# Kernel tuning notes

Measured on AMD Instinct MI355X. Metric: run time of the kernel, lower is better.

The kernel has to match this reference:

```python
import jax, jax.numpy as jnp
import numpy as np

# PGA G(3,0,1) basis order: [1, e0, e1, e2, e3, e01, e02, e03, e12, e13, e23, e012, e013, e023, e123, e0123].
# The invariant inner product <rev(x) y>_0 only involves blades NOT containing e0; for those blades
# the metric contribution is +1, so it is a plain dot product over these 8 components.
_IP_IDX = np.array([0, 2, 3, 4, 8, 9, 10, 14])
_EPS = 1e-3  # config.normalizer_eps


def _normalizer(x):
    # _lin_square_normalizer: x / (x^2 + eps), a bounded ~1/x-style transform
    return x / (x * x + _EPS)


def setup_inputs() -> dict:
    key = jax.random.key(0)
    ks = jax.random.split(key, 7)
    B, H, N, CMV, CS = 2, 8, 2048, 16, 32
    f = lambda k, s: jax.random.normal(k, s, dtype=jnp.float32)
    return {
        "q_mv": f(ks[0], (B, H, N, CMV, 16)),
        "k_mv": f(ks[1], (B, H, N, CMV, 16)),
        "v_mv": f(ks[2], (B, H, N, CMV, 16)),
        "q_s": f(ks[3], (B, H, N, CS)),
        "k_s": f(ks[4], (B, H, N, CS)),
        "v_s": f(ks[5], (B, H, N, CS)),
        "log_weights": 0.1 * f(ks[6], (H, 1, CMV)),
    }


def reference(q_mv, k_mv, v_mv, q_s, k_s, v_s, log_weights):
    B, H, N, CMV, _ = q_mv.shape
    CS = q_s.shape[-1]

    # per-head, per-mv-channel learned positive weights, broadcast over items and blades
    w = jnp.exp(log_weights)[None, :, :, :, None]  # (1, H, 1, CMV, 1)

    # Term 1: weighted PGA inner product of multivector q/k (8 non-degenerate blades per channel)
    q_ip = (q_mv[..., _IP_IDX] * w).reshape(B, H, N, CMV * 8)
    k_ip = k_mv[..., _IP_IDX].reshape(B, H, N, CMV * 8)

    # Term 2: transformed scalar inner product <phi(q_s), psi(k_s)> with phi=psi=normalizer
    # Term 3: Euclidean scalar inner product <q_s, k_s>
    q_feat = jnp.concatenate([q_ip, _normalizer(q_s), q_s], axis=-1)  # (B,H,N, 8*CMV + 2*CS)
    k_feat = jnp.concatenate([k_ip, _normalizer(k_s), k_s], axis=-1)

    scale = 1.0 / jnp.sqrt(jnp.asarray(q_feat.shape[-1], dtype=q_feat.dtype))
    scores = jnp.einsum("bhid,bhjd->bhij", q_feat, k_feat) * scale  # (B,H,N,N)
    attn = jax.nn.softmax(scores, axis=-1)

    # Shared attention weights applied to flattened multivector + scalar values
    v_flat = jnp.concatenate([v_mv.reshape(B, H, N, CMV * 16), v_s], axis=-1)  # (B,H,N, 16*CMV+CS)
    out = jnp.einsum("bhij,bhjd->bhid", attn, v_flat)

    out_mv = out[..., : CMV * 16].reshape(B, H, N, CMV, 16)
    out_s = out[..., CMV * 16 :]
    return out_mv, out_s
```

## Files before the change

kernel.cpp:

```cpp
#include <hip/hip_runtime.h>

typedef float f32x4 __attribute__((ext_vector_type(4)));
typedef _Float16 f16x8 __attribute__((ext_vector_type(8)));
typedef _Float16 f16x4 __attribute__((ext_vector_type(4)));

#define NSEQ 2048
#define KVBLK 64
#define NITER (NSEQ / KVBLK)
#define KFBYTES (KVBLK * 384)
#define VTBYTES (288 * 2 * KVBLK)
#define TILEB (KFBYTES + VTBYTES)
#define KFOFF 0
#define VTOFF KFBYTES
#define PSTRIDE 72
#define WS_NEED (16ull * NITER * TILEB)

#define SCALE_L2E 0.10411754f
#define DEFER_THR 11.0f

__device__ __forceinline__ void async_copy16(const void* g, void* l) {
    __builtin_amdgcn_global_load_lds((const __attribute__((address_space(1))) unsigned int*)g,
                                     (__attribute__((address_space(3))) unsigned int*)l, 16, 0, 0);
}

__global__ __launch_bounds__(256)
void prep_kf(const float* __restrict__ k_mv, const float* __restrict__ k_s,
             unsigned char* __restrict__ ws)
{
    constexpr int IPIDX[8] = {0, 2, 3, 4, 8, 9, 10, 14};
    const int head = blockIdx.x >> 5, kt = blockIdx.x & 31;
    unsigned char* tb = ws + (size_t)(head * NITER + kt) * TILEB + KFOFF;
    const int tid = threadIdx.x;
    #pragma unroll
    for (int rep = 0; rep < 6; ++rep) {
        const int t = rep * 256 + tid;
        const int j = t & 63, oct = t >> 6;
        const size_t row = (size_t)head * NSEQ + kt * KVBLK + j;
        float v[8];
        if (oct < 16) {
            const float* p = k_mv + (row * 16 + oct) * 16;
            #pragma unroll
            for (int i = 0; i < 8; ++i) v[i] = p[IPIDX[i]];
        } else if (oct < 20) {
            const f32x4* p4 = (const f32x4*)(k_s + row * 32 + (oct - 16) * 8);
            f32x4 a = p4[0], b = p4[1];
            #pragma unroll
            for (int i = 0; i < 8; ++i) {
                float x = (i < 4) ? a[i & 3] : b[i & 3];
                v[i] = x / (x * x + 1e-3f);
            }
        } else {
            const f32x4* p4 = (const f32x4*)(k_s + row * 32 + (oct - 20) * 8);
            f32x4 a = p4[0], b = p4[1];
            #pragma unroll
            for (int i = 0; i < 8; ++i) v[i] = (i < 4) ? a[i & 3] : b[i & 3];
        }
        f16x8 o;
        #pragma unroll
        for (int i = 0; i < 8; ++i) o[i] = (_Float16)v[i];
        *(f16x8*)(tb + ((j * 384 + oct * 16) ^ ((j & 7) << 4))) = o;
    }
}

__global__ __launch_bounds__(256)
void prep_vt(const float* __restrict__ v_mv, const float* __restrict__ v_s,
             unsigned char* __restrict__ ws)
{
    const int head = blockIdx.x >> 5, kt = blockIdx.x & 31;
    unsigned char* tb = ws + (size_t)(head * NITER + kt) * TILEB + VTOFF;
    const int tid = threadIdx.x;
    const size_t row0 = (size_t)head * NSEQ + kt * KVBLK;
    {
        const int d = tid;
        float val[KVBLK];
        #pragma unroll
        for (int j = 0; j < KVBLK; ++j) val[j] = v_mv[(row0 + j) * 256 + d];
        #pragma unroll
        for (int jg = 0; jg < 8; ++jg) {
            f16x8 o;
            #pragma unroll
            for (int i = 0; i < 8; ++i) o[i] = (_Float16)val[jg * 8 + i];
            *(f16x8*)(tb + ((d * 128 + jg * 16) ^ ((d & 7) << 4))) = o;
        }
    }
    if (tid < 32) {
        const int d = 256 + tid;
        float val[KVBLK];
        #pragma unroll
        for (int j = 0; j < KVBLK; ++j) val[j] = v_s[(row0 + j) * 32 + tid];
        #pragma unroll
        for (int jg = 0; jg < 8; ++jg) {
            f16x8 o;
            #pragma unroll
            for (int i = 0; i < 8; ++i) o[i] = (_Float16)val[jg * 8 + i];
            *(f16x8*)(tb + ((d * 128 + jg * 16) ^ ((d & 7) << 4))) = o;
        }
    }
}

__global__ __launch_bounds__(256, 2)
void geoattn_main(const float* __restrict__ q_mv, const float* __restrict__ q_s,
                  const float* __restrict__ logw, const unsigned char* __restrict__ ws,
                  float* __restrict__ out)
{
    constexpr int IPIDX[8] = {0, 2, 3, 4, 8, 9, 10, 14};
    __shared__ __align__(16) unsigned char lbuf[TILEB];
    __shared__ __align__(16) _Float16 P_all[4][16 * PSTRIDE];

    const int bid  = blockIdx.x;
    const int head = (bid & 7) | ((bid >> 8) << 3);
    const int qt   = (bid >> 3) & 31;
    const int h    = head & 7;

    const int tid  = threadIdx.x;
    const int w    = tid >> 6;
    const int lane = tid & 63;
    const int lr   = lane & 15;
    const int lg   = lane >> 4;

    const size_t rowbase = (size_t)head * NSEQ;
    const int q0 = qt * 64;
    const unsigned char* wsh = ws + (size_t)head * NITER * TILEB;

    #pragma unroll
    for (int c = 0; c < 15; ++c)
        async_copy16(wsh + c * 4096 + tid * 16, &lbuf[c * 4096 + tid * 16]);

    f16x8 qf[6];
    {
        const int qrow = q0 + w * 16 + lr;
        const float* qmv = q_mv + (rowbase + qrow) * 256;
        const float* qs  = q_s  + (rowbase + qrow) * 32;
        #pragma unroll
        for (int c = 0; c < 4; ++c) {
            const int cmv = 4 * c + lg;
            const float wgt = __expf(logw[h * 16 + cmv]) * SCALE_L2E;
            const float* p = qmv + cmv * 16;
            #pragma unroll
            for (int i = 0; i < 8; ++i)
                qf[c][i] = (_Float16)(p[IPIDX[i]] * wgt);
        }
        const f32x4* p4 = (const f32x4*)(qs + lg * 8);
        f32x4 a = p4[0], b = p4[1];
        #pragma unroll
        for (int i = 0; i < 8; ++i) {
            float x = (i < 4) ? a[i & 3] : b[i & 3];
            qf[4][i] = (_Float16)(SCALE_L2E * x / (x * x + 1e-3f));
            qf[5][i] = (_Float16)(SCALE_L2E * x);
        }
    }

    f32x4 acc[18];
    #pragma unroll
    for (int dt = 0; dt < 18; ++dt) acc[dt] = f32x4{0.f, 0.f, 0.f, 0.f};
    float mrun = -1e30f, lrun = 0.f;

    _Float16* pb = &P_all[w][0];

    asm volatile("s_waitcnt vmcnt(0)" ::: "memory");
    __builtin_amdgcn_s_barrier();
    asm volatile("" ::: "memory");

    for (int kt = 0; kt < NITER; ++kt) {
        f32x4 sacc[4];
        #pragma unroll
        for (int jt = 0; jt < 4; ++jt) sacc[jt] = f32x4{0.f, 0.f, 0.f, 0.f};
        __builtin_amdgcn_s_setprio(1);
        #pragma unroll
        for (int jt = 0; jt < 4; ++jt) {
            const int j = jt * 16 + lr;
            #pragma unroll
            for (int c = 0; c < 6; ++c) {
                f16x8 kf = *(const f16x8*)(lbuf + KFOFF +
                            ((j * 384 + c * 64 + lg * 16) ^ ((lr & 7) << 4)));
                sacc[jt] = __builtin_amdgcn_mfma_f32_16x16x32_f16(kf, qf[c], sacc[jt], 0, 0, 0);
            }
        }
        __builtin_amdgcn_s_setprio(0);

        float mloc;
        {
            float t0 = fmaxf(fmaxf(sacc[0][0], sacc[0][1]), fmaxf(sacc[0][2], sacc[0][3]));
            #pragma unroll
            for (int jt = 1; jt < 4; ++jt) {
                float t1 = fmaxf(fmaxf(sacc[jt][0], sacc[jt][1]), fmaxf(sacc[jt][2], sacc[jt][3]));
                t0 = fmaxf(t0, t1);
            }
            t0 = fmaxf(t0, __shfl_xor(t0, 16));
            t0 = fmaxf(t0, __shfl_xor(t0, 32));
            mloc = t0;
        }
        const bool need = (mloc > mrun + DEFER_THR);
        const float mnew = need ? mloc : mrun;
        const float alpha = exp2f(mrun - mnew);
        mrun = mnew;
        if (__ballot(need)) {
            float ar[4];
            #pragma unroll
            for (int r = 0; r < 4; ++r) ar[r] = __shfl(alpha, lg * 4 + r, 16);
            #pragma unroll
            for (int dt = 0; dt < 18; ++dt)
                #pragma unroll
                for (int r = 0; r < 4; ++r) acc[dt][r] *= ar[r];
            lrun *= alpha;
        }
        float ps = 0.f;
        #pragma unroll
        for (int jt = 0; jt < 4; ++jt) {
            f16x4 pk;
            #pragma unroll
            for (int r = 0; r < 4; ++r) {
                const float p = exp2f(sacc[jt][r] - mrun);
                ps += p;
                pk[r] = (_Float16)p;
            }
            *(f16x4*)(&pb[lr * PSTRIDE + jt * 16 + lg * 4]) = pk;
        }
        ps += __shfl_xor(ps, 16);
        ps += __shfl_xor(ps, 32);
        lrun += ps;

        f16x8 pf0 = *(const f16x8*)(&pb[lr * PSTRIDE + lg * 8]);
        f16x8 pf1 = *(const f16x8*)(&pb[lr * PSTRIDE + 32 + lg * 8]);
        __builtin_amdgcn_s_setprio(1);
        #pragma unroll
        for (int dt = 0; dt < 18; ++dt) {
            const int d = dt * 16 + lr;
            const int vb = VTOFF + d * 128 + lg * 16;
            f16x8 vf0 = *(const f16x8*)(lbuf + ((vb) ^ ((d & 7) << 4)));
            f16x8 vf1 = *(const f16x8*)(lbuf + ((vb + 64) ^ ((d & 7) << 4)));
            acc[dt] = __builtin_amdgcn_mfma_f32_16x16x32_f16(pf0, vf0, acc[dt], 0, 0, 0);
            acc[dt] = __builtin_amdgcn_mfma_f32_16x16x32_f16(pf1, vf1, acc[dt], 0, 0, 0);
        }
        __builtin_amdgcn_s_setprio(0);

        asm volatile("s_waitcnt lgkmcnt(0)" ::: "memory");
        __builtin_amdgcn_s_barrier();
        asm volatile("" ::: "memory");
        if (kt < NITER - 1) {
            const unsigned char* src = wsh + (size_t)(kt + 1) * TILEB;
            #pragma unroll
            for (int c = 0; c < 15; ++c)
                async_copy16(src + c * 4096 + tid * 16, &lbuf[c * 4096 + tid * 16]);
            asm volatile("s_waitcnt vmcnt(0)" ::: "memory");
            __builtin_amdgcn_s_barrier();
            asm volatile("" ::: "memory");
        }
    }

    #pragma unroll
    for (int r = 0; r < 4; ++r) {
        const float lv = __shfl(lrun, lg * 4 + r, 16);
        const float inv = 1.0f / lv;
        const int row = q0 + w * 16 + lg * 4 + r;
        float* omv = out + (rowbase + row) * 256;
        float* os  = out + 8388608ull + (rowbase + row) * 32;
        #pragma unroll
        for (int dt = 0; dt < 18; ++dt) {
            const int d = dt * 16 + lr;
            const float val = acc[dt][r] * inv;
            if (d < 256) omv[d] = val;
            else         os[d - 256] = val;
        }
    }
}

#define FKSTRIDE 200
#define FVSTRIDE 72
__global__ __launch_bounds__(256, 2)
void geoattn_fallback(const float* __restrict__ q_mv, const float* __restrict__ k_mv,
                      const float* __restrict__ v_mv, const float* __restrict__ q_s,
                      const float* __restrict__ k_s, const float* __restrict__ v_s,
                      const float* __restrict__ logw, float* __restrict__ out)
{
    constexpr int IPIDX[8] = {0, 2, 3, 4, 8, 9, 10, 14};
    __shared__ __align__(16) _Float16 lds_k[64 * FKSTRIDE];
    __shared__ __align__(16) _Float16 lds_vt[288 * FVSTRIDE];
    __shared__ __align__(16) _Float16 lds_p[4 * 16 * FVSTRIDE];

    const int bid  = blockIdx.x;
    const int head = (bid & 7) | ((bid >> 8) << 3);
    const int qt   = (bid >> 3) & 31;
    const int h    = head & 7;
    const int tid  = threadIdx.x;
    const int w    = tid >> 6;
    const int lane = tid & 63;
    const int lr   = lane & 15;
    const int lg   = lane >> 4;
    const size_t rowbase = (size_t)head * NSEQ;
    const int q0 = qt * 64;
    const float scale = 0.07216878364870323f;

    f16x8 qf[6];
    {
        const int qrow = q0 + w * 16 + lr;
        const float* qmv = q_mv + (rowbase + qrow) * 256;
        const float* qs  = q_s  + (rowbase + qrow) * 32;
        #pragma unroll
        for (int c = 0; c < 4; ++c) {
            const int cmv = 4 * c + lg;
            const float wgt = __expf(logw[h * 16 + cmv]) * scale;
            const float* p = qmv + cmv * 16;
            #pragma unroll
            for (int i = 0; i < 8; ++i) qf[c][i] = (_Float16)(p[IPIDX[i]] * wgt);
        }
        const f32x4* p4 = (const f32x4*)(qs + lg * 8);
        f32x4 a = p4[0], b = p4[1];
        #pragma unroll
        for (int i = 0; i < 8; ++i) {
            float x = (i < 4) ? a[i & 3] : b[i & 3];
            qf[4][i] = (_Float16)(scale * x / (x * x + 1e-3f));
            qf[5][i] = (_Float16)(scale * x);
        }
    }
    f32x4 acc[18];
    #pragma unroll
    for (int dt = 0; dt < 18; ++dt) acc[dt] = f32x4{0.f, 0.f, 0.f, 0.f};
    float mrun[4] = {-1e30f, -1e30f, -1e30f, -1e30f};
    float lrun[4] = {0.f, 0.f, 0.f, 0.f};

    for (int kt = 0; kt < 32; ++kt) {
        const int j0 = kt * 64;
        __syncthreads();
        #pragma unroll
        for (int rep = 0; rep < 6; ++rep) {
            const int t = rep * 256 + tid;
            const int j = t & 63, oct = t >> 6;
            const size_t krow = rowbase + j0 + j;
            float v[8];
            if (oct < 16) {
                const float* p = k_mv + (krow * 16 + oct) * 16;
                #pragma unroll
                for (int i = 0; i < 8; ++i) v[i] = p[IPIDX[i]];
            } else if (oct < 20) {
                const f32x4* p4 = (const f32x4*)(k_s + krow * 32 + (oct - 16) * 8);
                f32x4 a = p4[0], b = p4[1];
                #pragma unroll
                for (int i = 0; i < 8; ++i) {
                    float x = (i < 4) ? a[i & 3] : b[i & 3];
                    v[i] = x / (x * x + 1e-3f);
                }
            } else {
                const f32x4* p4 = (const f32x4*)(k_s + krow * 32 + (oct - 20) * 8);
                f32x4 a = p4[0], b = p4[1];
                #pragma unroll
                for (int i = 0; i < 8; ++i) v[i] = (i < 4) ? a[i & 3] : b[i & 3];
            }
            f16x8 o;
            #pragma unroll
            for (int i = 0; i < 8; ++i) o[i] = (_Float16)v[i];
            *(f16x8*)(&lds_k[j * FKSTRIDE + oct * 8]) = o;
        }
        #pragma unroll
        for (int rep = 0; rep < 9; ++rep) {
            const int t = rep * 256 + tid;
            const int j = t & 63, oct = t >> 6;
            const size_t vrow = rowbase + j0 + j;
            const float* src = (oct < 32) ? (v_mv + vrow * 256 + oct * 8)
                                          : (v_s  + vrow * 32 + (oct - 32) * 8);
            const f32x4* p4 = (const f32x4*)src;
            f32x4 a = p4[0], b = p4[1];
            const int d0 = oct * 8;
            #pragma unroll
            for (int i = 0; i < 8; ++i)
                lds_vt[(d0 + i) * FVSTRIDE + j] = (_Float16)((i < 4) ? a[i & 3] : b[i & 3]);
        }
        __syncthreads();
        f32x4 sacc[4];
        #pragma unroll
        for (int nt = 0; nt < 4; ++nt) {
            sacc[nt] = f32x4{0.f, 0.f, 0.f, 0.f};
            #pragma unroll
            for (int c = 0; c < 6; ++c) {
                f16x8 kf = *(const f16x8*)(&lds_k[(lr + 16 * nt) * FKSTRIDE + 32 * c + lg * 8]);
                sacc[nt] = __builtin_amdgcn_mfma_f32_16x16x32_f16(qf[c], kf, sacc[nt], 0, 0, 0);
            }
        }
        float tmax[4], alpha[4];
        #pragma unroll
        for (int r = 0; r < 4; ++r) {
            float t0 = fmaxf(fmaxf(sacc[0][r], sacc[1][r]), fmaxf(sacc[2][r], sacc[3][r]));
            #pragma unroll
            for (int mm = 1; mm < 16; mm <<= 1) t0 = fmaxf(t0, __shfl_xor(t0, mm));
            tmax[r] = t0;
        }
        bool need = false;
        #pragma unroll
        for (int r = 0; r < 4; ++r) {
            float mnew = fmaxf(mrun[r], tmax[r]);
            need = need || (tmax[r] > mrun[r]);
            alpha[r] = __expf(mrun[r] - mnew);
            mrun[r] = mnew;
        }
        float pvv[4][4];
        float psum[4] = {0.f, 0.f, 0.f, 0.f};
        #pragma unroll
        for (int nt = 0; nt < 4; ++nt)
            #pragma unroll
            for (int r = 0; r < 4; ++r) {
                float p = __expf(sacc[nt][r] - mrun[r]);
                pvv[nt][r] = p;
                psum[r] += p;
            }
        #pragma unroll
        for (int r = 0; r < 4; ++r) {
            float s = psum[r];
            #pragma unroll
            for (int mm = 1; mm < 16; mm <<= 1) s += __shfl_xor(s, mm);
            lrun[r] = lrun[r] * alpha[r] + s;
        }
        if (__ballot(need)) {
            #pragma unroll
            for (int dt = 0; dt < 18; ++dt)
                #pragma unroll
                for (int r = 0; r < 4; ++r) acc[dt][r] *= alpha[r];
        }
        _Float16* pbf = &lds_p[w * 16 * FVSTRIDE];
        #pragma unroll
        for (int nt = 0; nt < 4; ++nt)
            #pragma unroll
            for (int r = 0; r < 4; ++r)
                pbf[(lg * 4 + r) * FVSTRIDE + lr + 16 * nt] = (_Float16)pvv[nt][r];
        #pragma unroll
        for (int ch = 0; ch < 2; ++ch) {
            f16x8 pf = *(const f16x8*)(&pbf[lr * FVSTRIDE + 32 * ch + lg * 8]);
            #pragma unroll
            for (int dt = 0; dt < 18; ++dt) {
                f16x8 vf = *(const f16x8*)(&lds_vt[(lr + 16 * dt) * FVSTRIDE + 32 * ch + lg * 8]);
                acc[dt] = __builtin_amdgcn_mfma_f32_16x16x32_f16(pf, vf, acc[dt], 0, 0, 0);
            }
        }
    }
    const int orow = q0 + w * 16 + lg * 4;
    #pragma unroll
    for (int r = 0; r < 4; ++r) {
        const float inv = 1.0f / lrun[r];
        float* omv = out + (rowbase + orow + r) * 256;
        float* os  = out + 8388608ull + (rowbase + orow + r) * 32;
        #pragma unroll
        for (int dt = 0; dt < 18; ++dt) {
            const int d = lr + 16 * dt;
            const float val = acc[dt][r] * inv;
            if (d < 256) omv[d] = val;
            else         os[d - 256] = val;
        }
    }
}

extern "C" void kernel_launch(void* const* d_in, const int* in_sizes, int n_in,
                              void* d_out, int out_size, void* d_ws, size_t ws_size,
                              hipStream_t stream) {
    (void)in_sizes; (void)n_in; (void)out_size;
    const float* q_mv = (const float*)d_in[0];
    const float* k_mv = (const float*)d_in[1];
    const float* v_mv = (const float*)d_in[2];
    const float* q_s  = (const float*)d_in[3];
    const float* k_s  = (const float*)d_in[4];
    const float* v_s  = (const float*)d_in[5];
    const float* logw = (const float*)d_in[6];
    float* out = (float*)d_out;

    if (ws_size >= WS_NEED) {
        unsigned char* ws = (unsigned char*)d_ws;
        prep_kf<<<dim3(512), dim3(256), 0, stream>>>(k_mv, k_s, ws);
        prep_vt<<<dim3(512), dim3(256), 0, stream>>>(v_mv, v_s, ws);
        geoattn_main<<<dim3(512), dim3(256), 0, stream>>>(q_mv, q_s, logw, ws, out);
    } else {
        geoattn_fallback<<<dim3(512), dim3(256), 0, stream>>>(q_mv, k_mv, v_mv, q_s, k_s, v_s, logw, out);
    }
}
```

Baseline: 122.6 us.

## Stream V tiles from global into registers and keep only K in LDS

The main kernel now stages only the K-feature tile in LDS and loads the transposed V tile straight from global memory (L2) into registers, in three chunks spread across the QK, softmax and PV phases. The prefetch of the next K tile now starts right after the QK MFMAs instead of at the end of the iteration. The V layout in the workspace drops its XOR swizzle to match the direct global reads. This shrinks LDS per block and overlaps V fetch latency with compute, at the cost of many more vector registers for the V fragments and a reliance on L2 hits for V, since each head's V is reread by 32 query-tile blocks.

```diff
diff --git a/kernel.cpp b/kernel.cpp
--- a/kernel.cpp
+++ b/kernel.cpp
@@ -80,7 +80,7 @@
             f16x8 o;
             #pragma unroll
             for (int i = 0; i < 8; ++i) o[i] = (_Float16)val[jg * 8 + i];
-            *(f16x8*)(tb + ((d * 128 + jg * 16) ^ ((d & 7) << 4))) = o;
+            *(f16x8*)(tb + d * 128 + jg * 16) = o;
         }
     }
     if (tid < 32) {
@@ -93,7 +93,7 @@
             f16x8 o;
             #pragma unroll
             for (int i = 0; i < 8; ++i) o[i] = (_Float16)val[jg * 8 + i];
-            *(f16x8*)(tb + ((d * 128 + jg * 16) ^ ((d & 7) << 4))) = o;
+            *(f16x8*)(tb + d * 128 + jg * 16) = o;
         }
     }
 }
@@ -104,7 +104,7 @@
                   float* __restrict__ out)
 {
     constexpr int IPIDX[8] = {0, 2, 3, 4, 8, 9, 10, 14};
-    __shared__ __align__(16) unsigned char lbuf[TILEB];
+    __shared__ __align__(16) unsigned char lbuf[KFBYTES];
     __shared__ __align__(16) _Float16 P_all[4][16 * PSTRIDE];
 
     const int bid  = blockIdx.x;
@@ -123,8 +123,8 @@
     const unsigned char* wsh = ws + (size_t)head * NITER * TILEB;
 
     #pragma unroll
-    for (int c = 0; c < 15; ++c)
-        async_copy16(wsh + c * 4096 + tid * 16, &lbuf[c * 4096 + tid * 16]);
+    for (int c = 0; c < 6; ++c)
+        async_copy16(wsh + KFOFF + c * 4096 + tid * 16, &lbuf[c * 4096 + tid * 16]);
 
     f16x8 qf[6];
     {
@@ -157,11 +157,21 @@
 
     _Float16* pb = &P_all[w][0];
 
-    asm volatile("s_waitcnt vmcnt(0)" ::: "memory");
-    __builtin_amdgcn_s_barrier();
-    asm volatile("" ::: "memory");
-
     for (int kt = 0; kt < NITER; ++kt) {
+        asm volatile("s_waitcnt vmcnt(0)" ::: "memory");
+        __builtin_amdgcn_s_barrier();
+        asm volatile("" ::: "memory");
+
+        const unsigned char* vtile = wsh + (size_t)kt * TILEB + VTOFF;
+
+        f16x8 vA[6][2];
+        #pragma unroll
+        for (int dl = 0; dl < 6; ++dl) {
+            const int d = dl * 16 + lr;
+            vA[dl][0] = *(const f16x8*)(vtile + d * 128 + lg * 16);
+            vA[dl][1] = *(const f16x8*)(vtile + d * 128 + 64 + lg * 16);
+        }
+
         f32x4 sacc[4];
         #pragma unroll
         for (int jt = 0; jt < 4; ++jt) sacc[jt] = f32x4{0.f, 0.f, 0.f, 0.f};
@@ -177,6 +187,23 @@
             }
         }
         __builtin_amdgcn_s_setprio(0);
+
+        asm volatile("s_waitcnt lgkmcnt(0)" ::: "memory");
+        __builtin_amdgcn_s_barrier();
+        asm volatile("" ::: "memory");
+        if (kt < NITER - 1) {
+            const unsigned char* src = wsh + (size_t)(kt + 1) * TILEB + KFOFF;
+            #pragma unroll
+            for (int c = 0; c < 6; ++c)
+                async_copy16(src + c * 4096 + tid * 16, &lbuf[c * 4096 + tid * 16]);
+        }
+        f16x8 vB[6][2];
+        #pragma unroll
+        for (int dl = 0; dl < 6; ++dl) {
+            const int d = (6 + dl) * 16 + lr;
+            vB[dl][0] = *(const f16x8*)(vtile + d * 128 + lg * 16);
+            vB[dl][1] = *(const f16x8*)(vtile + d * 128 + 64 + lg * 16);
+        }
 
         float mloc;
         {
@@ -224,28 +251,30 @@
         f16x8 pf1 = *(const f16x8*)(&pb[lr * PSTRIDE + 32 + lg * 8]);
         __builtin_amdgcn_s_setprio(1);
         #pragma unroll
-        for (int dt = 0; dt < 18; ++dt) {
-            const int d = dt * 16 + lr;
-            const int vb = VTOFF + d * 128 + lg * 16;
-            f16x8 vf0 = *(const f16x8*)(lbuf + ((vb) ^ ((d & 7) << 4)));
-            f16x8 vf1 = *(const f16x8*)(lbuf + ((vb + 64) ^ ((d & 7) << 4)));
-            acc[dt] = __builtin_amdgcn_mfma_f32_16x16x32_f16(pf0, vf0, acc[dt], 0, 0, 0);
-            acc[dt] = __builtin_amdgcn_mfma_f32_16x16x32_f16(pf1, vf1, acc[dt], 0, 0, 0);
+        for (int dl = 0; dl < 6; ++dl) {
+            acc[dl] = __builtin_amdgcn_mfma_f32_16x16x32_f16(pf0, vA[dl][0], acc[dl], 0, 0, 0);
+            acc[dl] = __builtin_amdgcn_mfma_f32_16x16x32_f16(pf1, vA[dl][1], acc[dl], 0, 0, 0);
         }
         __builtin_amdgcn_s_setprio(0);
-
-        asm volatile("s_waitcnt lgkmcnt(0)" ::: "memory");
-        __builtin_amdgcn_s_barrier();
-        asm volatile("" ::: "memory");
-        if (kt < NITER - 1) {
-            const unsigned char* src = wsh + (size_t)(kt + 1) * TILEB;
-            #pragma unroll
-            for (int c = 0; c < 15; ++c)
-                async_copy16(src + c * 4096 + tid * 16, &lbuf[c * 4096 + tid * 16]);
-            asm volatile("s_waitcnt vmcnt(0)" ::: "memory");
-            __builtin_amdgcn_s_barrier();
-            asm volatile("" ::: "memory");
-        }
+        f16x8 vC[6][2];
+        #pragma unroll
+        for (int dl = 0; dl < 6; ++dl) {
+            const int d = (12 + dl) * 16 + lr;
+            vC[dl][0] = *(const f16x8*)(vtile + d * 128 + lg * 16);
+            vC[dl][1] = *(const f16x8*)(vtile + d * 128 + 64 + lg * 16);
+        }
+        __builtin_amdgcn_s_setprio(1);
+        #pragma unroll
+        for (int dl = 0; dl < 6; ++dl) {
+            acc[6 + dl] = __builtin_amdgcn_mfma_f32_16x16x32_f16(pf0, vB[dl][0], acc[6 + dl], 0, 0, 0);
+            acc[6 + dl] = __builtin_amdgcn_mfma_f32_16x16x32_f16(pf1, vB[dl][1], acc[6 + dl], 0, 0, 0);
+        }
+        #pragma unroll
+        for (int dl = 0; dl < 6; ++dl) {
+            acc[12 + dl] = __builtin_amdgcn_mfma_f32_16x16x32_f16(pf0, vC[dl][0], acc[12 + dl], 0, 0, 0);
+            acc[12 + dl] = __builtin_amdgcn_mfma_f32_16x16x32_f16(pf1, vC[dl][1], acc[12 + dl], 0, 0, 0);
+        }
+        __builtin_amdgcn_s_setprio(0);
     }
 
     #pragma unroll
```

New measurement: 311.8 us. 2.54x slower.
